# Performance work log

Measured on AMD Instinct MI355X. Metric: run time of the kernel, lower is better.

## Reference

```python
import jax, jax.numpy as jnp
import numpy as np

NEG_SLOPE = 0.1

def lrelu(x):
    return jnp.where(x >= 0, x, NEG_SLOPE * x)

def conv2d(x, w, b, padding=0, dilation=1):
    y = jax.lax.conv_general_dilated(
        x, w, window_strides=(1, 1),
        padding=[(padding, padding), (padding, padding)],
        rhs_dilation=(dilation, dilation),
        dimension_numbers=('NCHW', 'OIHW', 'NCHW'))
    return y + b[None, :, None, None]

def res_aspp(x, p):
    r1 = lrelu(conv2d(x, p['a1_w'], p['a1_b'], padding=1, dilation=1))
    r2 = lrelu(conv2d(x, p['a2_w'], p['a2_b'], padding=2, dilation=2))
    r3 = lrelu(conv2d(x, p['a3_w'], p['a3_b'], padding=4, dilation=4))
    r = conv2d(jnp.concatenate((r1, r2, r3), axis=1), p['ar_w'], p['ar_b'])
    return x + r

def deform_conv2d(x, offset, w, b):
    # x: [B,C,H,W], offset: [B,2*K,H,W] torchvision layout (y,x) per 3x3 tap
    B, C, H, W = x.shape
    KH = KW = 3
    K = KH * KW
    pad = 1
    off = offset.reshape(B, K, 2, H, W)
    ky, kx = jnp.meshgrid(jnp.arange(KH), jnp.arange(KW), indexing='ij')
    ky = ky.reshape(K).astype(x.dtype)
    kx = kx.reshape(K).astype(x.dtype)
    hh = jnp.arange(H, dtype=x.dtype)
    ww = jnp.arange(W, dtype=x.dtype)
    # sampling positions [B,K,H,W]
    py = off[:, :, 0] + (hh[None, None, :, None] - pad + ky[None, :, None, None])
    px = off[:, :, 1] + (ww[None, None, None, :] - pad + kx[None, :, None, None])
    y0 = jnp.floor(py)
    x0 = jnp.floor(px)
    wy = (py - y0)[:, None]  # [B,1,K,H,W]
    wx = (px - x0)[:, None]
    y0i = y0.astype(jnp.int32)
    x0i = x0.astype(jnp.int32)
    x_flat = x.reshape(B, C, H * W)

    def gather(iy, ix):
        valid = ((iy >= 0) & (iy < H) & (ix >= 0) & (ix < W)).astype(x.dtype)
        idx = jnp.clip(iy, 0, H - 1) * W + jnp.clip(ix, 0, W - 1)  # [B,K,H,W]
        v = jax.vmap(lambda xb, ib: xb[:, ib])(x_flat, idx.reshape(B, -1))
        return v.reshape(B, C, K, H, W) * valid[:, None]

    samp = (gather(y0i, x0i) * (1 - wy) * (1 - wx)
            + gather(y0i, x0i + 1) * (1 - wy) * wx
            + gather(y0i + 1, x0i) * wy * (1 - wx)
            + gather(y0i + 1, x0i + 1) * wy * wx)
    out = jnp.einsum('bckhw,ock->bohw', samp, w.reshape(w.shape[0], C, K))
    return out + b[None, :, None, None]

def setup_inputs() -> dict:
    key = jax.random.key(0)
    ks = jax.random.split(key, 16)
    B, C, H, W = 4, 64, 160, 160
    Cout = 64
    s = 0.05
    d = {
        'in_aux': jax.random.normal(ks[0], (B, C, H, W), jnp.float32),
        'in_ref': jax.random.normal(ks[1], (B, C, H, W), jnp.float32),
        'w01': jax.random.normal(ks[2], (Cout, 2 * C, 1, 1), jnp.float32) * s,
        'b01': jnp.zeros((Cout,), jnp.float32),
        'a1_w': jax.random.normal(ks[3], (Cout, Cout, 3, 3), jnp.float32) * s,
        'a1_b': jnp.zeros((Cout,), jnp.float32),
        'a2_w': jax.random.normal(ks[4], (Cout, Cout, 3, 3), jnp.float32) * s,
        'a2_b': jnp.zeros((Cout,), jnp.float32),
        'a3_w': jax.random.normal(ks[5], (Cout, Cout, 3, 3), jnp.float32) * s,
        'a3_b': jnp.zeros((Cout,), jnp.float32),
        'ar_w': jax.random.normal(ks[6], (Cout, 3 * Cout, 1, 1), jnp.float32) * s,
        'ar_b': jnp.zeros((Cout,), jnp.float32),
        'w02': jax.random.normal(ks[7], (18, Cout, 1, 1), jnp.float32) * s,
        'b02': jnp.zeros((18,), jnp.float32),
        'dw': jax.random.normal(ks[8], (Cout, C, 3, 3), jnp.float32) * s,
        'db': jnp.zeros((Cout,), jnp.float32),
    }
    return d

def reference(in_aux, in_ref, w01, b01, a1_w, a1_b, a2_w, a2_b, a3_w, a3_b,
              ar_w, ar_b, w02, b02, dw, db):
    cat_x = jnp.concatenate((in_aux, in_ref), axis=1)
    off_x = lrelu(conv2d(cat_x, w01, b01))
    p = {'a1_w': a1_w, 'a1_b': a1_b, 'a2_w': a2_w, 'a2_b': a2_b,
         'a3_w': a3_w, 'a3_b': a3_b, 'ar_w': ar_w, 'ar_b': ar_b}
    off_x = res_aspp(off_x, p)
    off_x = conv2d(off_x, w02, b02)
    return deform_conv2d(in_aux, off_x, dw, db)
```

## Files before the change

kernel.cpp:

```cpp
#include <hip/hip_runtime.h>
#include <math.h>

static constexpr int B = 4, H = 160, W = 160;
static constexpr int HW = H * W;
static constexpr int CHW = 64 * HW;
static constexpr int NELEM = B * CHW;

static constexpr int WP = 168;
static constexpr int HP = 168;
static constexpr int PHW = WP * HP;
static constexpr int PGUARD = 704;
static constexpr int PSTRIDE = 30720;
static constexpr int IMGOFS = PGUARD + 4 * WP + 4;

typedef short bf16x8 __attribute__((ext_vector_type(8)));
typedef float f32x4 __attribute__((ext_vector_type(4)));

__device__ __forceinline__ float lrelu(float v) { return v >= 0.f ? v : 0.1f * v; }

__device__ __forceinline__ unsigned short f2bf(float f) {
  unsigned u = __float_as_uint(f);
  return (unsigned short)((u + 0x7FFFu + ((u >> 16) & 1u)) >> 16);
}
__device__ __forceinline__ float bf2f(short u) {
  return __uint_as_float(((unsigned)(unsigned short)u) << 16);
}

__device__ __forceinline__ void glds16(const void* g, void* l) {
  __builtin_amdgcn_global_load_lds(
      (const __attribute__((address_space(1))) void*)g,
      (__attribute__((address_space(3))) void*)l, 16, 0, 0);
}

__global__ __launch_bounds__(256) void k_transform(
    const float* __restrict__ w01, const float* __restrict__ dw,
    const float* __restrict__ arw, const float* __restrict__ a1w,
    const float* __restrict__ a2w, const float* __restrict__ a3w,
    float* __restrict__ wt01, unsigned short* __restrict__ wb_bf,
    unsigned short* __restrict__ wd_bf, unsigned short* __restrict__ arw_bf,
    unsigned short* __restrict__ off0p) {
  int i = blockIdx.x * 256 + threadIdx.x;
  uint4* zp = (uint4*)off0p;
#pragma unroll
  for (int j = 0; j < 6; ++j) {
    unsigned u = (unsigned)i + (unsigned)j * 167936u;
    if (u < 983040u) zp[u] = make_uint4(0u, 0u, 0u, 0u);
  }
  if (i < 8192) {
    int ci = i >> 6, o = i & 63;
    wt01[i] = w01[o * 128 + ci];
  } else if (i < 118784) {
    int j = i - 8192;
    int ci = j & 63, co = (j >> 6) & 63;
    int kk = j >> 12;
    int dsel = kk / 9; kk -= dsel * 9;
    const float* src = dsel == 0 ? a1w : dsel == 1 ? a2w : a3w;
    wb_bf[j] = f2bf(src[(co * 64 + ci) * 9 + kk]);
  } else if (i < 155648) {
    int j = i - 118784;
    int ci = j & 63, co = (j >> 6) & 63, k = j >> 12;
    wd_bf[j] = f2bf(dw[(co * 64 + ci) * 9 + k]);
  } else if (i < 167936) {
    int j = i - 155648;
    arw_bf[j] = f2bf(arw[j]);
  }
}

__global__ __launch_bounds__(256) void k_conv1x1_in(
    const float* __restrict__ aux, const float* __restrict__ ref,
    const float* __restrict__ wt01, const float* __restrict__ b01,
    float* __restrict__ out, unsigned short* __restrict__ off0p,
    unsigned short* __restrict__ x_bf) {
  __shared__ float s[128 * 64];
  int pos0 = blockIdx.x * 64;
  int b = pos0 / HW;
  int hw0 = pos0 - b * HW;
  int tid = threadIdx.x;
  for (int i = tid; i < 8192; i += 256) {
    int ci = i >> 6, p = i & 63;
    const float* src = (ci < 64) ? (aux + b * CHW + ci * HW)
                                 : (ref + b * CHW + (ci - 64) * HW);
    s[i] = src[hw0 + p];
  }
  __syncthreads();
  int p = tid & 63;
  int g = __builtin_amdgcn_readfirstlane(tid >> 6);
  const float* wp = wt01 + g * 16;
  float acc[16];
#pragma unroll
  for (int j = 0; j < 16; ++j) acc[j] = 0.f;
#pragma unroll 4
  for (int ci = 0; ci < 128; ++ci) {
    float sv = s[ci * 64 + p];
    const float* wrow = wp + ci * 64;
#pragma unroll
    for (int j = 0; j < 16; ++j) acc[j] += sv * wrow[j];
  }
  const float* bb = b01 + g * 16;
  int obase = (b * 64 + g * 16) * HW + hw0 + p;
  unsigned short tb[16];
#pragma unroll
  for (int j = 0; j < 16; ++j) {
    float v = lrelu(acc[j] + bb[j]);
    out[obase + j * HW] = v;
    tb[j] = f2bf(v);
  }
  int hw = hw0 + p;
  int h = hw / W, w = hw - h * W;
  unsigned short* dst =
      off0p + ((size_t)b * PSTRIDE + IMGOFS + h * WP + w) * 64 + g * 16;
  *(uint4*)dst = *(const uint4*)&tb[0];
  *(uint4*)(dst + 8) = *(const uint4*)&tb[8];
  unsigned short xb[16];
#pragma unroll
  for (int j = 0; j < 16; ++j) xb[j] = f2bf(s[(g * 16 + j) * 64 + p]);
  unsigned short* xdst = x_bf + ((size_t)(b * HW + hw0 + p)) * 64 + g * 16;
  *(uint4*)xdst = *(const uint4*)&xb[0];
  *(uint4*)(xdst + 8) = *(const uint4*)&xb[8];
}

__global__ __launch_bounds__(256) void k_aspp3_mfma(
    const unsigned short* __restrict__ off0p,
    const unsigned short* __restrict__ wb_bf,
    const float* __restrict__ a1b, const float* __restrict__ a2b,
    const float* __restrict__ a3b, unsigned short* __restrict__ r_bf) {
  __shared__ unsigned short sa[2][288 * 64];
  int tid = threadIdx.x;
  int lane = tid & 63, wid = tid >> 6;
  int m = lane & 15, q = lane >> 4;

  int p0 = blockIdx.x;
  int xcd = p0 & 7, ii = p0 >> 3;
  int base = xcd < 4 ? xcd * 167 : 668 + (xcd - 4) * 166;
  int lid = base + ii;
  int dsel = lid % 3;
  int tj = lid / 3;
  int b = tj / 111;
  int tile = tj - b * 111;
  int pos0 = tile * 256;
  const int d = 1 << dsel;
  const unsigned short* pb = off0p + (size_t)b * PSTRIDE * 64;
  const float* bias = dsel == 0 ? a1b : dsel == 1 ? a2b : a3b;

  f32x4 acc[4][4] = {};

  auto STAGE = [&](int buf, int ky) {
    const char* src =
        (const char*)(pb + (size_t)(PGUARD + pos0 + (ky - 1) * d * WP - 16) * 64);
    char* dstb = (char*)&sa[buf][0];
#pragma unroll
    for (int r = 0; r < 9; ++r) {
      int X = r * 4096 + tid * 16;
      int row = X >> 7;
      int Xs = X ^ ((row & 7) << 4);
      glds16(src + Xs, dstb + X);
    }
  };
  auto COMPUTE = [&](int buf, int ky) {
    const char* sb = (const char*)&sa[buf][0];
#pragma unroll
    for (int kx = 0; kx < 3; ++kx) {
      const unsigned short* wk = wb_bf + (dsel * 9 + ky * 3 + kx) * 4096;
      int px0 = 16 + (kx - 1) * d + wid * 64;
#pragma unroll
      for (int kc = 0; kc < 2; ++kc) {
        bf16x8 bfrag[4];
#pragma unroll
        for (int t = 0; t < 4; ++t)
          bfrag[t] = *(const bf16x8*)(wk + (t * 16 + m) * 64 + kc * 32 + q * 8);
#pragma unroll
        for (int mt = 0; mt < 4; ++mt) {
          int px = px0 + mt * 16 + m;
          int byteoff = px * 128 + ((kc * 64 + q * 16) ^ ((px & 7) << 4));
          bf16x8 afrag = *(const bf16x8*)(sb + byteoff);
#pragma unroll
          for (int t = 0; t < 4; ++t)
            acc[mt][t] = __builtin_amdgcn_mfma_f32_16x16x32_bf16(
                afrag, bfrag[t], acc[mt][t], 0, 0, 0);
        }
      }
    }
  };

  STAGE(0, 0);
  __syncthreads();
  STAGE(1, 1);
  COMPUTE(0, 0);
  __syncthreads();
  STAGE(0, 2);
  COMPUTE(1, 1);
  __syncthreads();
  COMPUTE(0, 2);

  __syncthreads();
  unsigned short* epb = &sa[0][0];
#pragma unroll
  for (int t = 0; t < 4; ++t) {
    float bi = bias[t * 16 + m];
#pragma unroll
    for (int mt = 0; mt < 4; ++mt)
#pragma unroll
      for (int r = 0; r < 4; ++r)
        epb[(wid * 64 + mt * 16 + q * 4 + r) * 68 + t * 16 + m] =
            f2bf(lrelu(acc[mt][t][r] + bi));
  }
  __syncthreads();
  {
    int qa = pos0 + tid;
    int pr = qa / WP, pc = qa - pr * WP;
    if (pr >= 4 && pr < 164 && pc >= 4 && pc < 164) {
      int hw = (pr - 4) * W + (pc - 4);
      unsigned short* dst = r_bf + ((size_t)(b * HW + hw)) * 192 + dsel * 64;
      const unsigned short* s2 = epb + tid * 68;
#pragma unroll
      for (int c = 0; c < 8; ++c)
        *(uint4*)(dst + c * 8) = *(const uint4*)(s2 + c * 8);
    }
  }
}

__global__ __launch_bounds__(256) void k_merge_head_mfma(
    const unsigned short* __restrict__ r_bf, const float* __restrict__ off0,
    const unsigned short* __restrict__ arw_bf, const float* __restrict__ arb,
    const float* __restrict__ w02, const float* __restrict__ b02,
    float* __restrict__ offs) {
  __shared__ unsigned short sa[64 * 200];
  int pos0 = blockIdx.x * 64;
  int b = pos0 / HW;
  int hw0 = pos0 - b * HW;
  int tid = threadIdx.x;
  const unsigned short* gsrc = r_bf + (size_t)(b * HW + hw0) * 192;
  for (int i = tid; i < 1536; i += 256) {
    int pos = i / 24, c8 = i - pos * 24;
    *(uint4*)(sa + pos * 200 + c8 * 8) = *(const uint4*)(gsrc + i * 8);
  }
  __syncthreads();
  int lane = tid & 63, wid = tid >> 6;
  int m = lane & 15, q = lane >> 4;
  f32x4 acc[4] = {};
#pragma unroll
  for (int kc = 0; kc < 6; ++kc) {
    bf16x8 bfrag = *(const bf16x8*)(arw_bf + (wid * 16 + m) * 192 + kc * 32 + q * 8);
#pragma unroll
    for (int mt = 0; mt < 4; ++mt) {
      bf16x8 afrag = *(const bf16x8*)(sa + (mt * 16 + m) * 200 + kc * 32 + q * 8);
      acc[mt] = __builtin_amdgcn_mfma_f32_16x16x32_bf16(afrag, bfrag, acc[mt],
                                                        0, 0, 0);
    }
  }
  __syncthreads();
  float* ep = (float*)sa;
  int co = wid * 16 + m;
  float bi = arb[co];
  const float* resrow = off0 + (size_t)(b * 64 + co) * HW + hw0;
#pragma unroll
  for (int mt = 0; mt < 4; ++mt)
#pragma unroll
    for (int r = 0; r < 4; ++r) {
      int pos = mt * 16 + q * 4 + r;
      ep[pos * 65 + co] = acc[mt][r] + bi + resrow[pos];
    }
  __syncthreads();
  for (int i = tid; i < 1152; i += 256) {
    int t = i >> 6, p = i & 63;
    const float* w2 = w02 + t * 64;
    float o = b02[t];
#pragma unroll 8
    for (int c = 0; c < 64; ++c) o += ep[p * 65 + c] * w2[c];
    offs[(b * 18 + t) * HW + hw0 + p] = o;
  }
}

__global__ __launch_bounds__(256) void k_deform_mfma(
    const unsigned short* __restrict__ x_bf, const float* __restrict__ offs,
    const unsigned short* __restrict__ wd_bf, const float* __restrict__ db,
    float* __restrict__ out) {
  constexpr int SP = 72;
  __shared__ unsigned short sb[2][64 * SP];
  int blk = (blockIdx.x & 7) * 200 + (blockIdx.x >> 3);
  int pos0 = blk * 64;
  int b = pos0 / HW;
  int hw0 = pos0 - b * HW;
  int tid = threadIdx.x;
  int lane = tid & 63, wid = tid >> 6;
  int m = lane & 15, q = lane >> 4;
  int p = lane;
  int cg = wid;
  int hw = hw0 + p;
  int h = hw / W, wv = hw - h * W;
  const unsigned short* xb = x_bf + (size_t)b * HW * 64;
  const float* ob = offs + b * 18 * HW + hw;
  float offv[18];
#pragma unroll
  for (int j = 0; j < 18; ++j) offv[j] = ob[j * HW];
  f32x4 acc[4] = {};

#pragma unroll
  for (int k = 0; k < 9; ++k) {
    const int ky = k / 3, kx = k - ky * 3;
    float py = offv[2 * k] + (float)(h - 1 + ky);
    float px = offv[2 * k + 1] + (float)(wv - 1 + kx);
    float fy = floorf(py), fx = floorf(px);
    int iy0 = (int)fy, ix0 = (int)fx;
    float wy = py - fy, wx = px - fx;
    int iy1 = iy0 + 1, ix1 = ix0 + 1;
    float vy0 = (iy0 >= 0 && iy0 < H) ? 1.f : 0.f;
    float vy1 = (iy1 >= 0 && iy1 < H) ? 1.f : 0.f;
    float vx0 = (ix0 >= 0 && ix0 < W) ? 1.f : 0.f;
    float vx1 = (ix1 >= 0 && ix1 < W) ? 1.f : 0.f;
    int cy0 = min(max(iy0, 0), H - 1), cy1 = min(max(iy1, 0), H - 1);
    int cx0 = min(max(ix0, 0), W - 1), cx1 = min(max(ix1, 0), W - 1);
    float c00 = vy0 * vx0 * (1.f - wy) * (1.f - wx);
    float c01 = vy0 * vx1 * (1.f - wy) * wx;
    float c10 = vy1 * vx0 * wy * (1.f - wx);
    float c11 = vy1 * vx1 * wy * wx;
    const unsigned short* p00 = xb + (size_t)(cy0 * W + cx0) * 64 + cg * 16;
    const unsigned short* p01 = xb + (size_t)(cy0 * W + cx1) * 64 + cg * 16;
    const unsigned short* p10 = xb + (size_t)(cy1 * W + cx0) * 64 + cg * 16;
    const unsigned short* p11 = xb + (size_t)(cy1 * W + cx1) * 64 + cg * 16;
    unsigned short tb[16];
#pragma unroll
    for (int c2 = 0; c2 < 2; ++c2) {
      bf16x8 v00 = *(const bf16x8*)(p00 + c2 * 8);
      bf16x8 v01 = *(const bf16x8*)(p01 + c2 * 8);
      bf16x8 v10 = *(const bf16x8*)(p10 + c2 * 8);
      bf16x8 v11 = *(const bf16x8*)(p11 + c2 * 8);
#pragma unroll
      for (int j = 0; j < 8; ++j) {
        float sv = c00 * bf2f(v00[j]) + c01 * bf2f(v01[j]) +
                   c10 * bf2f(v10[j]) + c11 * bf2f(v11[j]);
        tb[c2 * 8 + j] = f2bf(sv);
      }
    }
    unsigned short* wr = &sb[k & 1][p * SP + cg * 16];
    *(uint4*)wr = *(const uint4*)&tb[0];
    *(uint4*)(wr + 8) = *(const uint4*)&tb[8];
    __syncthreads();
    const unsigned short* rb = &sb[k & 1][0];
#pragma unroll
    for (int kc = 0; kc < 2; ++kc) {
      bf16x8 bfrag =
          *(const bf16x8*)(wd_bf + (k * 64 + wid * 16 + m) * 64 + kc * 32 + q * 8);
#pragma unroll
      for (int mt = 0; mt < 4; ++mt) {
        bf16x8 afrag = *(const bf16x8*)(rb + (mt * 16 + m) * SP + kc * 32 + q * 8);
        acc[mt] = __builtin_amdgcn_mfma_f32_16x16x32_bf16(afrag, bfrag, acc[mt],
                                                          0, 0, 0);
      }
    }
  }
  int co = wid * 16 + m;
  float bias = db[co];
  size_t orow = (size_t)(b * 64 + co) * HW + hw0;
#pragma unroll
  for (int mt = 0; mt < 4; ++mt)
#pragma unroll
    for (int r = 0; r < 4; ++r)
      out[orow + mt * 16 + q * 4 + r] = acc[mt][r] + bias;
}

extern "C" void kernel_launch(void* const* d_in, const int* in_sizes, int n_in,
                              void* d_out, int out_size, void* d_ws, size_t ws_size,
                              hipStream_t stream) {
  const float* aux = (const float*)d_in[0];
  const float* ref = (const float*)d_in[1];
  const float* w01 = (const float*)d_in[2];
  const float* b01 = (const float*)d_in[3];
  const float* a1w = (const float*)d_in[4];
  const float* a1b = (const float*)d_in[5];
  const float* a2w = (const float*)d_in[6];
  const float* a2b = (const float*)d_in[7];
  const float* a3w = (const float*)d_in[8];
  const float* a3b = (const float*)d_in[9];
  const float* arw = (const float*)d_in[10];
  const float* arb = (const float*)d_in[11];
  const float* w02 = (const float*)d_in[12];
  const float* b02 = (const float*)d_in[13];
  const float* dw  = (const float*)d_in[14];
  const float* db  = (const float*)d_in[15];
  float* out = (float*)d_out;

  float* off0 = (float*)d_ws;
  float* offs = off0 + NELEM;
  float* wt01 = offs + B * 18 * HW;
  unsigned short* off0p = (unsigned short*)(wt01 + 8192);
  unsigned short* x_bf   = off0p + (size_t)B * PSTRIDE * 64;
  unsigned short* wb_bf  = x_bf + (size_t)NELEM;
  unsigned short* wd_bf  = wb_bf + 110592;
  unsigned short* arw_bf = wd_bf + 36864;
  unsigned short* r_bf   = arw_bf + 12288;

  k_transform<<<656, 256, 0, stream>>>(w01, dw, arw, a1w, a2w, a3w,
                                       wt01, wb_bf, wd_bf, arw_bf, off0p);
  k_conv1x1_in<<<B * HW / 64, 256, 0, stream>>>(aux, ref, wt01, b01, off0,
                                                off0p, x_bf);
  k_aspp3_mfma<<<1332, 256, 0, stream>>>(off0p, wb_bf, a1b, a2b, a3b, r_bf);
  k_merge_head_mfma<<<B * HW / 64, 256, 0, stream>>>(
      r_bf, off0, arw_bf, arb, w02, b02, offs);
  k_deform_mfma<<<B * HW / 64, 256, 0, stream>>>(x_bf, offs, wd_bf, db, out);
}
```

Before: 328.9 us.

## Restructure deform conv: 32-pixel tiles, gather all taps then MFMA once

The deformable conv kernel now handles 32 output pixels per block instead of 64, doubling the grid. Each wave handles 16 channels as two 8-channel halves across lanes. All 9 taps are sampled into a single XOR-swizzled shared buffer before one barrier, so the per-tap syncthreads go away. The bilinear results are packed with v_cvt_pk_bf16_f32 instead of manual rounding. This trades more shared memory (36KB) and duplicated weight-fragment loads per block for more parallelism, fewer barriers and fewer bank conflicts.

Measured after the change: 333.5 us. About the same (+1.4%).

```diff
diff --git a/kernel.cpp b/kernel.cpp
--- a/kernel.cpp
+++ b/kernel.cpp
@@ -275,25 +275,24 @@
     const unsigned short* __restrict__ x_bf, const float* __restrict__ offs,
     const unsigned short* __restrict__ wd_bf, const float* __restrict__ db,
     float* __restrict__ out) {
-  constexpr int SP = 72;
-  __shared__ unsigned short sb[2][64 * SP];
-  int blk = (blockIdx.x & 7) * 200 + (blockIdx.x >> 3);
-  int pos0 = blk * 64;
+  __shared__ unsigned short smp[288 * 64];
+  int blk = (blockIdx.x & 7) * 400 + (blockIdx.x >> 3);
+  int pos0 = blk * 32;
   int b = pos0 / HW;
   int hw0 = pos0 - b * HW;
   int tid = threadIdx.x;
   int lane = tid & 63, wid = tid >> 6;
   int m = lane & 15, q = lane >> 4;
-  int p = lane;
-  int cg = wid;
-  int hw = hw0 + p;
+  int sp = lane & 31;
+  int ch8 = lane >> 5;
+  int cbyte = wid * 32 + ch8 * 16;
+  int hw = hw0 + sp;
   int h = hw / W, wv = hw - h * W;
-  const unsigned short* xb = x_bf + (size_t)b * HW * 64;
+  const unsigned short* xbase = x_bf + (size_t)b * HW * 64 + wid * 16 + ch8 * 8;
   const float* ob = offs + b * 18 * HW + hw;
   float offv[18];
 #pragma unroll
   for (int j = 0; j < 18; ++j) offv[j] = ob[j * HW];
-  f32x4 acc[4] = {};
 
 #pragma unroll
   for (int k = 0; k < 9; ++k) {
@@ -314,46 +313,47 @@
     float c01 = vy0 * vx1 * (1.f - wy) * wx;
     float c10 = vy1 * vx0 * wy * (1.f - wx);
     float c11 = vy1 * vx1 * wy * wx;
-    const unsigned short* p00 = xb + (size_t)(cy0 * W + cx0) * 64 + cg * 16;
-    const unsigned short* p01 = xb + (size_t)(cy0 * W + cx1) * 64 + cg * 16;
-    const unsigned short* p10 = xb + (size_t)(cy1 * W + cx0) * 64 + cg * 16;
-    const unsigned short* p11 = xb + (size_t)(cy1 * W + cx1) * 64 + cg * 16;
-    unsigned short tb[16];
-#pragma unroll
-    for (int c2 = 0; c2 < 2; ++c2) {
-      bf16x8 v00 = *(const bf16x8*)(p00 + c2 * 8);
-      bf16x8 v01 = *(const bf16x8*)(p01 + c2 * 8);
-      bf16x8 v10 = *(const bf16x8*)(p10 + c2 * 8);
-      bf16x8 v11 = *(const bf16x8*)(p11 + c2 * 8);
-#pragma unroll
-      for (int j = 0; j < 8; ++j) {
-        float sv = c00 * bf2f(v00[j]) + c01 * bf2f(v01[j]) +
-                   c10 * bf2f(v10[j]) + c11 * bf2f(v11[j]);
-        tb[c2 * 8 + j] = f2bf(sv);
-      }
-    }
-    unsigned short* wr = &sb[k & 1][p * SP + cg * 16];
-    *(uint4*)wr = *(const uint4*)&tb[0];
-    *(uint4*)(wr + 8) = *(const uint4*)&tb[8];
-    __syncthreads();
-    const unsigned short* rb = &sb[k & 1][0];
+    bf16x8 v00 = *(const bf16x8*)(xbase + (size_t)(cy0 * W + cx0) * 64);
+    bf16x8 v01 = *(const bf16x8*)(xbase + (size_t)(cy0 * W + cx1) * 64);
+    bf16x8 v10 = *(const bf16x8*)(xbase + (size_t)(cy1 * W + cx0) * 64);
+    bf16x8 v11 = *(const bf16x8*)(xbase + (size_t)(cy1 * W + cx1) * 64);
+    unsigned tw[4];
+#pragma unroll
+    for (int jj = 0; jj < 4; ++jj) {
+      float s0 = c00 * bf2f(v00[2 * jj]) + c01 * bf2f(v01[2 * jj]) +
+                 c10 * bf2f(v10[2 * jj]) + c11 * bf2f(v11[2 * jj]);
+      float s1 = c00 * bf2f(v00[2 * jj + 1]) + c01 * bf2f(v01[2 * jj + 1]) +
+                 c10 * bf2f(v10[2 * jj + 1]) + c11 * bf2f(v11[2 * jj + 1]);
+      asm("v_cvt_pk_bf16_f32 %0, %1, %2" : "=v"(tw[jj]) : "v"(s0), "v"(s1));
+    }
+    int row = k * 32 + sp;
+    char* dst = (char*)smp + row * 128 + (cbyte ^ ((row & 7) << 4));
+    *(uint4*)dst = *(const uint4*)&tw[0];
+  }
+  __syncthreads();
+
+  f32x4 acc[2] = {};
+#pragma unroll
+  for (int k = 0; k < 9; ++k)
 #pragma unroll
     for (int kc = 0; kc < 2; ++kc) {
-      bf16x8 bfrag =
-          *(const bf16x8*)(wd_bf + (k * 64 + wid * 16 + m) * 64 + kc * 32 + q * 8);
-#pragma unroll
-      for (int mt = 0; mt < 4; ++mt) {
-        bf16x8 afrag = *(const bf16x8*)(rb + (mt * 16 + m) * SP + kc * 32 + q * 8);
+      bf16x8 bfrag = *(const bf16x8*)(wd_bf + (k * 64 + wid * 16 + m) * 64 +
+                                      kc * 32 + q * 8);
+#pragma unroll
+      for (int mt = 0; mt < 2; ++mt) {
+        int row = k * 32 + mt * 16 + m;
+        int off = (kc * 64 + q * 16) ^ ((row & 7) << 4);
+        bf16x8 afrag = *(const bf16x8*)((const char*)smp + row * 128 + off);
         acc[mt] = __builtin_amdgcn_mfma_f32_16x16x32_bf16(afrag, bfrag, acc[mt],
                                                           0, 0, 0);
       }
     }
-  }
+
   int co = wid * 16 + m;
   float bias = db[co];
   size_t orow = (size_t)(b * 64 + co) * HW + hw0;
 #pragma unroll
-  for (int mt = 0; mt < 4; ++mt)
+  for (int mt = 0; mt < 2; ++mt)
 #pragma unroll
     for (int r = 0; r < 4; ++r)
       out[orow + mt * 16 + q * 4 + r] = acc[mt][r] + bias;
@@ -397,5 +397,5 @@
   k_aspp3_mfma<<<1332, 256, 0, stream>>>(off0p, wb_bf, a1b, a2b, a3b, r_bf);
   k_merge_head_mfma<<<B * HW / 64, 256, 0, stream>>>(
       r_bf, off0, arw_bf, arb, w02, b02, offs);
-  k_deform_mfma<<<B * HW / 64, 256, 0, stream>>>(x_bf, offs, wd_bf, db, out);
-}
+  k_deform_mfma<<<B * HW / 32, 256, 0, stream>>>(x_bf, offs, wd_bf, db, out);
+}
```

## Pair deformable taps per barrier, swizzle LDS tiles, pack bf16 converts, raise MFMA priority

Applied to the files above, without the earlier changes.

The deformable-conv kernel now samples two taps into separate LDS buffers before each barrier, which halves the number of block barriers and gives more gather loads in flight per sync. The padded LDS layout is replaced by an XOR-swizzled 128-byte-row layout to avoid bank conflicts without padding. The float-to-bf16 rounding is done with the packed v_cvt_pk_bf16_f32 instruction. s_setprio is raised around the MFMA sections in both the ASPP conv kernel and the deform kernel. LDS use doubles to 32 KB and the barrier is hand-coded, so correctness relies on the double buffering across iterations being safe.

New measurement: 323.3 us. About the same (-1.7%).

```diff
diff --git a/kernel.cpp b/kernel.cpp
--- a/kernel.cpp
+++ b/kernel.cpp
@@ -158,6 +158,7 @@
   };
   auto COMPUTE = [&](int buf, int ky) {
     const char* sb = (const char*)&sa[buf][0];
+    __builtin_amdgcn_s_setprio(1);
 #pragma unroll
     for (int kx = 0; kx < 3; ++kx) {
       const unsigned short* wk = wb_bf + (dsel * 9 + ky * 3 + kx) * 4096;
@@ -180,6 +181,7 @@
         }
       }
     }
+    __builtin_amdgcn_s_setprio(0);
   };
 
   STAGE(0, 0);
@@ -275,8 +277,7 @@
     const unsigned short* __restrict__ x_bf, const float* __restrict__ offs,
     const unsigned short* __restrict__ wd_bf, const float* __restrict__ db,
     float* __restrict__ out) {
-  constexpr int SP = 72;
-  __shared__ unsigned short sb[2][64 * SP];
+  __shared__ unsigned short sb[2][2][64 * 64];
   int blk = (blockIdx.x & 7) * 200 + (blockIdx.x >> 3);
   int pos0 = blk * 64;
   int b = pos0 / HW;
@@ -288,21 +289,20 @@
   int cg = wid;
   int hw = hw0 + p;
   int h = hw / W, wv = hw - h * W;
-  const unsigned short* xb = x_bf + (size_t)b * HW * 64;
+  const unsigned short* xbase = x_bf + (size_t)b * HW * 64;
   const float* ob = offs + b * 18 * HW + hw;
   float offv[18];
 #pragma unroll
   for (int j = 0; j < 18; ++j) offv[j] = ob[j * HW];
   f32x4 acc[4] = {};
 
-#pragma unroll
-  for (int k = 0; k < 9; ++k) {
+  auto SAMPLE = [&](int k, unsigned short* dstbase) {
     const int ky = k / 3, kx = k - ky * 3;
     float py = offv[2 * k] + (float)(h - 1 + ky);
-    float px = offv[2 * k + 1] + (float)(wv - 1 + kx);
-    float fy = floorf(py), fx = floorf(px);
+    float pxf = offv[2 * k + 1] + (float)(wv - 1 + kx);
+    float fy = floorf(py), fx = floorf(pxf);
     int iy0 = (int)fy, ix0 = (int)fx;
-    float wy = py - fy, wx = px - fx;
+    float wy = py - fy, wx = pxf - fx;
     int iy1 = iy0 + 1, ix1 = ix0 + 1;
     float vy0 = (iy0 >= 0 && iy0 < H) ? 1.f : 0.f;
     float vy1 = (iy1 >= 0 && iy1 < H) ? 1.f : 0.f;
@@ -314,41 +314,69 @@
     float c01 = vy0 * vx1 * (1.f - wy) * wx;
     float c10 = vy1 * vx0 * wy * (1.f - wx);
     float c11 = vy1 * vx1 * wy * wx;
-    const unsigned short* p00 = xb + (size_t)(cy0 * W + cx0) * 64 + cg * 16;
-    const unsigned short* p01 = xb + (size_t)(cy0 * W + cx1) * 64 + cg * 16;
-    const unsigned short* p10 = xb + (size_t)(cy1 * W + cx0) * 64 + cg * 16;
-    const unsigned short* p11 = xb + (size_t)(cy1 * W + cx1) * 64 + cg * 16;
-    unsigned short tb[16];
+    const unsigned short* p00 = xbase + (size_t)(cy0 * W + cx0) * 64 + cg * 16;
+    const unsigned short* p01 = xbase + (size_t)(cy0 * W + cx1) * 64 + cg * 16;
+    const unsigned short* p10 = xbase + (size_t)(cy1 * W + cx0) * 64 + cg * 16;
+    const unsigned short* p11 = xbase + (size_t)(cy1 * W + cx1) * 64 + cg * 16;
+    unsigned tw0[4], tw1[4];
 #pragma unroll
     for (int c2 = 0; c2 < 2; ++c2) {
       bf16x8 v00 = *(const bf16x8*)(p00 + c2 * 8);
       bf16x8 v01 = *(const bf16x8*)(p01 + c2 * 8);
       bf16x8 v10 = *(const bf16x8*)(p10 + c2 * 8);
       bf16x8 v11 = *(const bf16x8*)(p11 + c2 * 8);
-#pragma unroll
-      for (int j = 0; j < 8; ++j) {
-        float sv = c00 * bf2f(v00[j]) + c01 * bf2f(v01[j]) +
-                   c10 * bf2f(v10[j]) + c11 * bf2f(v11[j]);
-        tb[c2 * 8 + j] = f2bf(sv);
+      unsigned* tw = c2 ? tw1 : tw0;
+#pragma unroll
+      for (int jj = 0; jj < 4; ++jj) {
+        float s0 = c00 * bf2f(v00[2 * jj]) + c01 * bf2f(v01[2 * jj]) +
+                   c10 * bf2f(v10[2 * jj]) + c11 * bf2f(v11[2 * jj]);
+        float s1 = c00 * bf2f(v00[2 * jj + 1]) + c01 * bf2f(v01[2 * jj + 1]) +
+                   c10 * bf2f(v10[2 * jj + 1]) + c11 * bf2f(v11[2 * jj + 1]);
+        asm("v_cvt_pk_bf16_f32 %0, %1, %2" : "=v"(tw[jj]) : "v"(s0), "v"(s1));
       }
     }
-    unsigned short* wr = &sb[k & 1][p * SP + cg * 16];
-    *(uint4*)wr = *(const uint4*)&tb[0];
-    *(uint4*)(wr + 8) = *(const uint4*)&tb[8];
-    __syncthreads();
-    const unsigned short* rb = &sb[k & 1][0];
+    char* wbase = (char*)dstbase + p * 128;
+    *(uint4*)(wbase + ((cg * 32) ^ ((p & 7) << 4))) = *(const uint4*)&tw0[0];
+    *(uint4*)(wbase + ((cg * 32 + 16) ^ ((p & 7) << 4))) = *(const uint4*)&tw1[0];
+  };
+  auto GEMM_TAP = [&](int k, const unsigned short* basep) {
 #pragma unroll
     for (int kc = 0; kc < 2; ++kc) {
       bf16x8 bfrag =
           *(const bf16x8*)(wd_bf + (k * 64 + wid * 16 + m) * 64 + kc * 32 + q * 8);
 #pragma unroll
       for (int mt = 0; mt < 4; ++mt) {
-        bf16x8 afrag = *(const bf16x8*)(rb + (mt * 16 + m) * SP + kc * 32 + q * 8);
+        int row = mt * 16 + m;
+        int off = (kc * 64 + q * 16) ^ ((row & 7) << 4);
+        bf16x8 afrag = *(const bf16x8*)((const char*)basep + row * 128 + off);
         acc[mt] = __builtin_amdgcn_mfma_f32_16x16x32_bf16(afrag, bfrag, acc[mt],
                                                           0, 0, 0);
       }
     }
-  }
+  };
+
+#pragma unroll
+  for (int r = 0; r < 4; ++r) {
+    SAMPLE(2 * r, &sb[r & 1][0][0]);
+    SAMPLE(2 * r + 1, &sb[r & 1][1][0]);
+    __builtin_amdgcn_sched_barrier(0);
+    asm volatile("s_waitcnt lgkmcnt(0)" ::: "memory");
+    __builtin_amdgcn_s_barrier();
+    __builtin_amdgcn_sched_barrier(0);
+    __builtin_amdgcn_s_setprio(1);
+    GEMM_TAP(2 * r, &sb[r & 1][0][0]);
+    GEMM_TAP(2 * r + 1, &sb[r & 1][1][0]);
+    __builtin_amdgcn_s_setprio(0);
+  }
+  SAMPLE(8, &sb[0][0][0]);
+  __builtin_amdgcn_sched_barrier(0);
+  asm volatile("s_waitcnt lgkmcnt(0)" ::: "memory");
+  __builtin_amdgcn_s_barrier();
+  __builtin_amdgcn_sched_barrier(0);
+  __builtin_amdgcn_s_setprio(1);
+  GEMM_TAP(8, &sb[0][0][0]);
+  __builtin_amdgcn_s_setprio(0);
+
   int co = wid * 16 + m;
   float bias = db[co];
   size_t orow = (size_t)(b * 64 + co) * HW + hw0;
```
